# Kernel optimization log

Hardware: AMD Instinct MI355X
Metric: run time of the kernel (lower is better)

The kernel has to match this reference:

```python
import jax, jax.numpy as jnp
import numpy as np

B, S, D, H = 2, 2048, 1024, 16
HD = D // H  # 64
LN_EPS = 1e-5


def setup_inputs() -> dict:
    key = jax.random.key(0)
    ks = jax.random.split(key, 5)
    hidden_states = jax.random.normal(ks[0], (B, S, D), dtype=jnp.float32)
    attention_mask = jnp.zeros((B, 1, 1, S), dtype=jnp.float32)  # additive mask
    # LayerNorm params
    ln_gamma = jnp.ones((D,), dtype=jnp.float32)
    ln_beta = jnp.zeros((D,), dtype=jnp.float32)
    # Q/K/V projections, no bias; stored as [in, out]
    sc = 1.0 / np.sqrt(D)
    Wq = jax.random.normal(ks[1], (D, D), dtype=jnp.float32) * sc
    Wk = jax.random.normal(ks[2], (D, D), dtype=jnp.float32) * sc
    Wv = jax.random.normal(ks[3], (D, D), dtype=jnp.float32) * sc
    return {"hidden_states": hidden_states, "attention_mask": attention_mask,
            "ln_gamma": ln_gamma, "ln_beta": ln_beta, "Wq": Wq, "Wk": Wk, "Wv": Wv}


def _layernorm(x, g, b):
    mu = jnp.mean(x, axis=-1, keepdims=True)
    var = jnp.mean(jnp.square(x - mu), axis=-1, keepdims=True)
    return (x - mu) * jax.lax.rsqrt(var + LN_EPS) * g + b


def reference(hidden_states, attention_mask, ln_gamma, ln_beta, Wq, Wk, Wv):
    h = _layernorm(hidden_states, ln_gamma, ln_beta)          # [B,S,D]
    # project and split heads: [B,S,D] -> [B,H,S,HD]
    def split_heads(x):
        return x.reshape(B, S, H, HD).transpose(0, 2, 1, 3)
    q = split_heads(h @ Wq)
    k = split_heads(h @ Wk)
    v = split_heads(h @ Wv)
    scores = jnp.einsum('bhqd,bhkd->bhqk', q, k) / jnp.sqrt(jnp.float32(HD))
    scores = scores + attention_mask                           # additive mask broadcast
    probs = jax.nn.softmax(scores, axis=-1)                    # dropout p=0 -> identity
    ctx = jnp.einsum('bhqk,bhkd->bhqd', probs, v)              # [B,H,S,HD]
    ctx = ctx.transpose(0, 2, 1, 3).reshape(B, S, H * HD)      # [B,S,D]
    return ctx
```

## Files before the change

### kernel.cpp

```cpp
#include <hip/hip_runtime.h>
#include <hip/hip_bf16.h>
#include <cstdint>

#define B_ 2
#define S_ 2048
#define D_ 1024
#define H_ 16
#define HD_ 64
#define M_ (B_*S_)

#define LOG2E 1.4426950408889634f
#define C1_ (0.125f * LOG2E)

typedef unsigned short u16;
typedef __bf16 bf16x8 __attribute__((ext_vector_type(8)));
typedef u16 u16x8 __attribute__((ext_vector_type(8)));
typedef float f32x4 __attribute__((ext_vector_type(4)));
typedef float f32x16 __attribute__((ext_vector_type(16)));
typedef int i32x4 __attribute__((ext_vector_type(4)));

static __device__ __forceinline__ u16 f2bu(float f) {
  __bf16 b = (__bf16)f;
  return __builtin_bit_cast(unsigned short, b);
}

static __device__ __forceinline__ int cvtpk(float a, float b) {
  int r;
  asm("v_cvt_pk_bf16_f32 %0, %1, %2" : "=v"(r) : "v"(a), "v"(b));
  return r;
}
static __device__ __forceinline__ void plswap(int &x, int &y) {
  asm("v_permlane32_swap_b32 %0, %1" : "+v"(x), "+v"(y));
}

#define GLOAD16(g, l) __builtin_amdgcn_global_load_lds( \
    (__attribute__((address_space(1))) void*)(g), \
    (__attribute__((address_space(3))) void*)(l), 16, 0, 0)

__global__ __launch_bounds__(256) void ln_kernel(const float* __restrict__ x,
    const float* __restrict__ g, const float* __restrict__ be, u16* __restrict__ h) {
  const int row = blockIdx.x;
  const int t = threadIdx.x;
  float4 v = reinterpret_cast<const float4*>(x + (size_t)row * D_)[t];
  float s = v.x + v.y + v.z + v.w;
  float sq = v.x*v.x + v.y*v.y + v.z*v.z + v.w*v.w;
  #pragma unroll
  for (int off = 32; off >= 1; off >>= 1) {
    s  += __shfl_down(s, off);
    sq += __shfl_down(sq, off);
  }
  __shared__ float red[8];
  const int wave = t >> 6, lane = t & 63;
  if (lane == 0) { red[wave] = s; red[4 + wave] = sq; }
  __syncthreads();
  if (t == 0) {
    float ts = red[0]+red[1]+red[2]+red[3];
    float tq = red[4]+red[5]+red[6]+red[7];
    float mu = ts * (1.0f / D_);
    red[0] = mu;
    red[1] = rsqrtf(tq * (1.0f / D_) - mu*mu + 1e-5f);
  }
  __syncthreads();
  const float mu = red[0], rs = red[1];
  float4 gg = reinterpret_cast<const float4*>(g)[t];
  float4 bb = reinterpret_cast<const float4*>(be)[t];
  ushort4 o;
  o.x = f2bu((v.x - mu) * rs * gg.x + bb.x);
  o.y = f2bu((v.y - mu) * rs * gg.y + bb.y);
  o.z = f2bu((v.z - mu) * rs * gg.z + bb.z);
  o.w = f2bu((v.w - mu) * rs * gg.w + bb.w);
  reinterpret_cast<ushort4*>(h + (size_t)row * D_)[t] = o;
}

__global__ __launch_bounds__(256) void wt_kernel(const float* __restrict__ W0,
    const float* __restrict__ W1, const float* __restrict__ W2, u16* __restrict__ wt) {
  const int z = blockIdx.z;
  const float* W = (z == 0) ? W0 : ((z == 1) ? W1 : W2);
  u16* out = wt + (size_t)z * D_ * D_;
  __shared__ float tile[32][33];
  const int n0 = blockIdx.x * 32, k0 = blockIdx.y * 32;
  const int tx = threadIdx.x, ty = threadIdx.y;
  #pragma unroll
  for (int j = 0; j < 4; ++j)
    tile[ty + 8*j][tx] = W[(size_t)(k0 + ty + 8*j) * D_ + n0 + tx];
  __syncthreads();
  #pragma unroll
  for (int j = 0; j < 4; ++j)
    out[(size_t)(n0 + ty + 8*j) * D_ + k0 + tx] = f2bu(tile[tx][ty + 8*j]);
}

__global__ __launch_bounds__(256) void qkv_gemm(const u16* __restrict__ hbuf,
    const u16* __restrict__ wt, u16* __restrict__ qkv) {
  const int z = blockIdx.z;
  const u16* Bt = wt + (size_t)z * D_ * D_;
  u16* outp = qkv + (size_t)z * (B_*H_*S_*HD_);
  __shared__ __align__(16) u16 As[128 * 32];
  __shared__ __align__(16) u16 Bs[128 * 32];
  const int t = threadIdx.x, lane = t & 63, wave = t >> 6;
  const int row0 = blockIdx.y * 128, col0 = blockIdx.x * 128;
  const int wm = wave >> 1, wn = wave & 1;
  f32x4 acc[4][4] = {};
  const int schunk = (t & 3) ^ ((t >> 3) & 3);
  const u16* ag = hbuf + (size_t)(row0 + (t >> 2)) * D_ + schunk * 8;
  const u16* bg = Bt   + (size_t)(col0 + (t >> 2)) * D_ + schunk * 8;
  u16* lA = &As[wave * 512];
  u16* lB = &Bs[wave * 512];
  const char* Ac = (const char*)As;
  const char* Bc = (const char*)Bs;
  const int cbase = (((lane >> 4) ^ ((lane >> 1) & 3)) << 4);

  for (int k0 = 0; k0 < D_; k0 += 32) {
    GLOAD16(ag + k0,           lA);
    GLOAD16(ag + k0 + 64 * D_, lA + 2048);
    GLOAD16(bg + k0,           lB);
    GLOAD16(bg + k0 + 64 * D_, lB + 2048);
    __syncthreads();
    bf16x8 af[4], bfr[4];
    #pragma unroll
    for (int m = 0; m < 4; ++m)
      af[m] = *reinterpret_cast<const bf16x8*>(Ac + (wm*64 + m*16 + (lane & 15)) * 64 + cbase);
    #pragma unroll
    for (int n = 0; n < 4; ++n)
      bfr[n] = *reinterpret_cast<const bf16x8*>(Bc + (wn*64 + n*16 + (lane & 15)) * 64 + cbase);
    #pragma unroll
    for (int m = 0; m < 4; ++m) {
      #pragma unroll
      for (int n = 0; n < 4; ++n)
        acc[m][n] = __builtin_amdgcn_mfma_f32_16x16x32_bf16(af[m], bfr[n], acc[m][n], 0, 0, 0);
    }
    __syncthreads();
  }
  const float scl = (z == 0) ? C1_ : 1.0f;
  #pragma unroll
  for (int m = 0; m < 4; ++m) {
    #pragma unroll
    for (int n = 0; n < 4; ++n) {
      const int gcol = col0 + wn*64 + n*16 + (lane & 15);
      const int hI = gcol >> 6, dI = gcol & 63;
      #pragma unroll
      for (int r = 0; r < 4; ++r) {
        const int grow = row0 + wm*64 + m*16 + (lane >> 4) * 4 + r;
        const int bI = grow >> 11, sI = grow & (S_ - 1);
        size_t idx;
        if (z == 2) idx = ((size_t)(bI * H_ + hI) * HD_ + dI) * S_ + sI;
        else        idx = ((size_t)(bI * H_ + hI) * S_ + sI) * HD_ + dI;
        outp[idx] = f2bu(acc[m][n][r] * scl);
      }
    }
  }
}

static __device__ __forceinline__ void sm_pack(
    const f32x16& s, const float4* __restrict__ mk,
    float& dm, float& lsum, f32x16& o0, f32x16& o1,
    bf16x8& pfA, bf16x8& pfB) {
  float zb[16];
  #pragma unroll
  for (int r = 0; r < 4; ++r) {
    zb[r]      = s[r]      + ((const float*)&mk[0])[r];
    zb[r + 4]  = s[r + 4]  + ((const float*)&mk[1])[r];
    zb[r + 8]  = s[r + 8]  + ((const float*)&mk[2])[r];
    zb[r + 12] = s[r + 12] + ((const float*)&mk[3])[r];
  }
  float a0 = fmaxf(fmaxf(zb[0], zb[1]), zb[2]);
  float a1 = fmaxf(fmaxf(zb[3], zb[4]), zb[5]);
  float a2 = fmaxf(fmaxf(zb[6], zb[7]), zb[8]);
  float a3 = fmaxf(fmaxf(zb[9], zb[10]), zb[11]);
  float a4 = fmaxf(fmaxf(zb[12], zb[13]), zb[14]);
  float tm = fmaxf(fmaxf(fmaxf(a0, a1), fmaxf(a2, a3)), fmaxf(a4, zb[15]));
  if (__builtin_expect(__any(tm > dm + 8.0f), 0)) {
    float tp = fmaxf(tm, __shfl_xor(tm, 32));
    float dnew = fmaxf(dm, tp - 8.0f);
    float sf = __builtin_amdgcn_exp2f(dm - dnew);
    lsum *= sf; o0 = o0 * sf; o1 = o1 * sf; dm = dnew;
  }
  float p[16];
  #pragma unroll
  for (int r = 0; r < 16; ++r) p[r] = __builtin_amdgcn_exp2f(zb[r] - dm);
  float s01 = (p[0] + p[1]) + (p[2] + p[3]);
  float s23 = (p[4] + p[5]) + (p[6] + p[7]);
  float s45 = (p[8] + p[9]) + (p[10] + p[11]);
  float s67 = (p[12] + p[13]) + (p[14] + p[15]);
  lsum += (s01 + s23) + (s45 + s67);
  int pk01 = cvtpk(p[0], p[1]),   pk23 = cvtpk(p[2], p[3]);
  int pk45 = cvtpk(p[4], p[5]),   pk67 = cvtpk(p[6], p[7]);
  int pk89 = cvtpk(p[8], p[9]),   pkAB = cvtpk(p[10], p[11]);
  int pkCD = cvtpk(p[12], p[13]), pkEF = cvtpk(p[14], p[15]);
  plswap(pk01, pk45); plswap(pk23, pk67);
  plswap(pk89, pkCD); plswap(pkAB, pkEF);
  i32x4 c0 = {pk01, pk23, pk45, pk67};
  i32x4 c1 = {pk89, pkAB, pkCD, pkEF};
  pfA = __builtin_bit_cast(bf16x8, c0);
  pfB = __builtin_bit_cast(bf16x8, c1);
}

__global__ __launch_bounds__(256, 2) void attn_kernel(const u16* __restrict__ qkv,
    const float* __restrict__ mask, float* __restrict__ out) {
  const int bid = blockIdx.x;
  const int x = bid & 7, rr = bid >> 3;
  const int j = rr & 15;
  const int pidx = x + ((rr >> 4) << 3);
  const int hI = pidx & 15, bI = pidx >> 4;
  const size_t plane = (size_t)pidx * (S_ * HD_);
  const u16* Qp  = qkv + plane;
  const u16* Kp  = qkv + (size_t)(B_*H_*S_*HD_) + plane;
  const u16* Vtp = qkv + 2*(size_t)(B_*H_*S_*HD_) + plane;

  const int t = threadIdx.x, lane = t & 63, wave = t >> 6;
  const int cl = lane & 31, hf = lane >> 5;
  const int x7 = cl & 7;
  const int hx16 = (hf ^ x7) << 4;
  const int rg = (cl >> 3) * 1056 + x7 * 128;

  __shared__ __align__(16) u16 KsBuf[2][4224];
  __shared__ __align__(16) u16 VsBuf[2][4224];
  __shared__ float maskLds[S_];

  #pragma unroll
  for (int i = 0; i < 2; ++i) {
    float4 mv = reinterpret_cast<const float4*>(mask + (size_t)bI * S_)[t + i*256];
    float4 sm = {mv.x * LOG2E - 8.0f, mv.y * LOG2E - 8.0f,
                 mv.z * LOG2E - 8.0f, mv.w * LOG2E - 8.0f};
    reinterpret_cast<float4*>(maskLds)[t + i*256] = sm;
  }

  const int q0 = j * 128 + wave * 32;
  bf16x8 qf[4];
  #pragma unroll
  for (int d = 0; d < 4; ++d)
    qf[d] = *reinterpret_cast<const bf16x8*>(
        Qp + (size_t)(q0 + cl) * HD_ + d * 16 + hf * 8);

  const int sr = t >> 3;
  const int scol = ((t & 7) ^ ((t >> 3) & 7)) << 3;
  const u16* kSrc = Kp  + (size_t)sr * HD_ + scol;
  const u16* vSrc = Vtp + (size_t)sr * S_  + scol;
  const int dst0 = wave * 528, dst1 = (4 + wave) * 528;

  f32x16 oacc0 = {}, oacc1 = {};
  float dm = 0.f, lsum = 0.f;

  GLOAD16(kSrc,                   &KsBuf[0][dst0]);
  GLOAD16(kSrc + 32 * HD_,        &KsBuf[0][dst1]);
  GLOAD16(vSrc,                   &VsBuf[0][dst0]);
  GLOAD16(vSrc + 32 * (size_t)S_, &VsBuf[0][dst1]);
  int cur = 0;

  for (int kv0 = 0; kv0 < S_; kv0 += 64) {
    __syncthreads();
    if (kv0 + 64 < S_) {
      const u16* kn = kSrc + (size_t)(kv0 + 64) * HD_;
      const u16* vn = vSrc + (kv0 + 64);
      GLOAD16(kn,                   &KsBuf[cur ^ 1][dst0]);
      GLOAD16(kn + 32 * HD_,        &KsBuf[cur ^ 1][dst1]);
      GLOAD16(vn,                   &VsBuf[cur ^ 1][dst0]);
      GLOAD16(vn + 32 * (size_t)S_, &VsBuf[cur ^ 1][dst1]);
    }
    const char* Ks = (const char*)KsBuf[cur];
    const char* Vs = (const char*)VsBuf[cur];

    bf16x8 k0[4], k1[4];
    #pragma unroll
    for (int d = 0; d < 4; ++d) {
      k0[d] = *reinterpret_cast<const bf16x8*>(Ks + rg + ((d << 5) ^ hx16));
      k1[d] = *reinterpret_cast<const bf16x8*>(Ks + rg + 4224 + ((d << 5) ^ hx16));
    }
    float4 mk0[4], mk1[4];
    #pragma unroll
    for (int i = 0; i < 4; ++i) {
      mk0[i] = *reinterpret_cast<const float4*>(&maskLds[kv0 + 8*i + 4*hf]);
      mk1[i] = *reinterpret_cast<const float4*>(&maskLds[kv0 + 32 + 8*i + 4*hf]);
    }
    f32x16 s0 = {}, s1 = {};
    __builtin_amdgcn_s_setprio(1);
    #pragma unroll
    for (int d = 0; d < 4; ++d)
      s0 = __builtin_amdgcn_mfma_f32_32x32x16_bf16(k0[d], qf[d], s0, 0, 0, 0);
    #pragma unroll
    for (int d = 0; d < 4; ++d)
      s1 = __builtin_amdgcn_mfma_f32_32x32x16_bf16(k1[d], qf[d], s1, 0, 0, 0);
    __builtin_amdgcn_s_setprio(0);

    bf16x8 v0[4], v1[4];
    v0[0] = *reinterpret_cast<const bf16x8*>(Vs + rg + (0 ^ hx16));
    v0[1] = *reinterpret_cast<const bf16x8*>(Vs + rg + 4224 + (0 ^ hx16));
    v0[2] = *reinterpret_cast<const bf16x8*>(Vs + rg + (32 ^ hx16));
    v0[3] = *reinterpret_cast<const bf16x8*>(Vs + rg + 4224 + (32 ^ hx16));
    bf16x8 pA, pB;
    sm_pack(s0, mk0, dm, lsum, oacc0, oacc1, pA, pB);
    __builtin_amdgcn_s_setprio(1);
    oacc0 = __builtin_amdgcn_mfma_f32_32x32x16_bf16(v0[0], pA, oacc0, 0, 0, 0);
    oacc1 = __builtin_amdgcn_mfma_f32_32x32x16_bf16(v0[1], pA, oacc1, 0, 0, 0);
    oacc0 = __builtin_amdgcn_mfma_f32_32x32x16_bf16(v0[2], pB, oacc0, 0, 0, 0);
    oacc1 = __builtin_amdgcn_mfma_f32_32x32x16_bf16(v0[3], pB, oacc1, 0, 0, 0);
    __builtin_amdgcn_s_setprio(0);
    v1[0] = *reinterpret_cast<const bf16x8*>(Vs + rg + (64 ^ hx16));
    v1[1] = *reinterpret_cast<const bf16x8*>(Vs + rg + 4224 + (64 ^ hx16));
    v1[2] = *reinterpret_cast<const bf16x8*>(Vs + rg + (96 ^ hx16));
    v1[3] = *reinterpret_cast<const bf16x8*>(Vs + rg + 4224 + (96 ^ hx16));
    sm_pack(s1, mk1, dm, lsum, oacc0, oacc1, pA, pB);
    __builtin_amdgcn_s_setprio(1);
    oacc0 = __builtin_amdgcn_mfma_f32_32x32x16_bf16(v1[0], pA, oacc0, 0, 0, 0);
    oacc1 = __builtin_amdgcn_mfma_f32_32x32x16_bf16(v1[1], pA, oacc1, 0, 0, 0);
    oacc0 = __builtin_amdgcn_mfma_f32_32x32x16_bf16(v1[2], pB, oacc0, 0, 0, 0);
    oacc1 = __builtin_amdgcn_mfma_f32_32x32x16_bf16(v1[3], pB, oacc1, 0, 0, 0);
    __builtin_amdgcn_s_setprio(0);
    cur ^= 1;
  }

  lsum += __shfl_xor(lsum, 32);
  const float rinv = 1.0f / lsum;
  float* orow = out + ((size_t)bI * S_ + q0 + cl) * D_ + hI * HD_;
  #pragma unroll
  for (int jj = 0; jj < 4; ++jj) {
    float4 o0 = {oacc0[4*jj] * rinv, oacc0[4*jj+1] * rinv, oacc0[4*jj+2] * rinv, oacc0[4*jj+3] * rinv};
    float4 o1 = {oacc1[4*jj] * rinv, oacc1[4*jj+1] * rinv, oacc1[4*jj+2] * rinv, oacc1[4*jj+3] * rinv};
    *reinterpret_cast<float4*>(orow + 8*jj + 4*hf)      = o0;
    *reinterpret_cast<float4*>(orow + 32 + 8*jj + 4*hf) = o1;
  }
}

extern "C" void kernel_launch(void* const* d_in, const int* in_sizes, int n_in,
                              void* d_out, int out_size, void* d_ws, size_t ws_size,
                              hipStream_t stream) {
  const float* x     = (const float*)d_in[0];
  const float* mask  = (const float*)d_in[1];
  const float* gamma = (const float*)d_in[2];
  const float* beta  = (const float*)d_in[3];
  const float* Wq    = (const float*)d_in[4];
  const float* Wk    = (const float*)d_in[5];
  const float* Wv    = (const float*)d_in[6];
  float* out = (float*)d_out;

  char* ws = (char*)d_ws;
  u16* hbuf = (u16*)ws;
  u16* wt   = (u16*)(ws + (size_t)M_*D_*2);
  u16* qkv  = (u16*)(ws + (size_t)M_*D_*2 + 3ull*D_*D_*2);

  hipLaunchKernelGGL(ln_kernel, dim3(M_), dim3(256), 0, stream, x, gamma, beta, hbuf);
  hipLaunchKernelGGL(wt_kernel, dim3(32, 32, 3), dim3(32, 8), 0, stream, Wq, Wk, Wv, wt);
  hipLaunchKernelGGL(qkv_gemm, dim3(8, 32, 3), dim3(256), 0, stream, hbuf, wt, qkv);
  hipLaunchKernelGGL(attn_kernel, dim3(512), dim3(256), 0, stream, qkv, mask, out);
}
```

Baseline: 106.9 us.

## Split attention KV range across two wave groups and merge partial softmax results

The attention block grows to 512 threads, made of two 4-wave groups. Each group processes half of the key/value sequence with its own double-buffered LDS tiles held in dynamic shared memory. At the end, group 1 writes its partial accumulators, row sum and max to LDS, and group 0 rescales and merges them before writing the output. This doubles the waves per block so more MFMA and latency-hiding parallelism is available on the 512-block grid, at the cost of more LDS per block (about 74KB), an extra merge step with two barriers, and possibly lower block occupancy.

```diff
diff --git a/kernel.cpp b/kernel.cpp
--- a/kernel.cpp
+++ b/kernel.cpp
@@ -194,8 +194,14 @@
   pfB = __builtin_bit_cast(bf16x8, c1);
 }
 
-__global__ __launch_bounds__(256, 2) void attn_kernel(const u16* __restrict__ qkv,
+__global__ __launch_bounds__(512, 4) void attn_kernel(const u16* __restrict__ qkv,
     const float* __restrict__ mask, float* __restrict__ out) {
+  extern __shared__ __align__(16) char shmem[];
+  char* Kbase = shmem;
+  char* Vbase = shmem + 33792;
+  float* maskLds = (float*)(shmem + 67584);
+  float* comb = (float*)shmem;
+
   const int bid = blockIdx.x;
   const int x = bid & 7, rr = bid >> 3;
   const int j = rr & 15;
@@ -207,57 +213,57 @@
   const u16* Vtp = qkv + 2*(size_t)(B_*H_*S_*HD_) + plane;
 
   const int t = threadIdx.x, lane = t & 63, wave = t >> 6;
+  const int g = wave >> 2, w4 = wave & 3;
   const int cl = lane & 31, hf = lane >> 5;
   const int x7 = cl & 7;
   const int hx16 = (hf ^ x7) << 4;
   const int rg = (cl >> 3) * 1056 + x7 * 128;
 
-  __shared__ __align__(16) u16 KsBuf[2][4224];
-  __shared__ __align__(16) u16 VsBuf[2][4224];
-  __shared__ float maskLds[S_];
-
-  #pragma unroll
-  for (int i = 0; i < 2; ++i) {
-    float4 mv = reinterpret_cast<const float4*>(mask + (size_t)bI * S_)[t + i*256];
+  {
+    float4 mv = reinterpret_cast<const float4*>(mask + (size_t)bI * S_)[t];
     float4 sm = {mv.x * LOG2E - 8.0f, mv.y * LOG2E - 8.0f,
                  mv.z * LOG2E - 8.0f, mv.w * LOG2E - 8.0f};
-    reinterpret_cast<float4*>(maskLds)[t + i*256] = sm;
-  }
-
-  const int q0 = j * 128 + wave * 32;
+    reinterpret_cast<float4*>(maskLds)[t] = sm;
+  }
+
+  const int q0 = j * 128 + w4 * 32;
   bf16x8 qf[4];
   #pragma unroll
   for (int d = 0; d < 4; ++d)
     qf[d] = *reinterpret_cast<const bf16x8*>(
         Qp + (size_t)(q0 + cl) * HD_ + d * 16 + hf * 8);
 
-  const int sr = t >> 3;
-  const int scol = ((t & 7) ^ ((t >> 3) & 7)) << 3;
-  const u16* kSrc = Kp  + (size_t)sr * HD_ + scol;
-  const u16* vSrc = Vtp + (size_t)sr * S_  + scol;
-  const int dst0 = wave * 528, dst1 = (4 + wave) * 528;
+  const int t8 = t & 255;
+  const int sr = t8 >> 3;
+  const int scol = ((t8 & 7) ^ (sr & 7)) << 3;
+  const u16* kSrc = Kp  + (size_t)(g * 1024 + sr) * HD_ + scol;
+  const u16* vSrc = Vtp + (size_t)sr * S_ + g * 1024 + scol;
+  char* kDst = Kbase + g * 16896 + w4 * 1056;
+  char* vDst = Vbase + g * 16896 + w4 * 1056;
 
   f32x16 oacc0 = {}, oacc1 = {};
   float dm = 0.f, lsum = 0.f;
 
-  GLOAD16(kSrc,                   &KsBuf[0][dst0]);
-  GLOAD16(kSrc + 32 * HD_,        &KsBuf[0][dst1]);
-  GLOAD16(vSrc,                   &VsBuf[0][dst0]);
-  GLOAD16(vSrc + 32 * (size_t)S_, &VsBuf[0][dst1]);
+  GLOAD16(kSrc,                   kDst);
+  GLOAD16(kSrc + 32 * HD_,        kDst + 4224);
+  GLOAD16(vSrc,                   vDst);
+  GLOAD16(vSrc + 32 * (size_t)S_, vDst + 4224);
   int cur = 0;
 
-  for (int kv0 = 0; kv0 < S_; kv0 += 64) {
+  for (int kv0 = 0; kv0 < 1024; kv0 += 64) {
     __syncthreads();
-    if (kv0 + 64 < S_) {
+    if (kv0 + 64 < 1024) {
       const u16* kn = kSrc + (size_t)(kv0 + 64) * HD_;
       const u16* vn = vSrc + (kv0 + 64);
-      GLOAD16(kn,                   &KsBuf[cur ^ 1][dst0]);
-      GLOAD16(kn + 32 * HD_,        &KsBuf[cur ^ 1][dst1]);
-      GLOAD16(vn,                   &VsBuf[cur ^ 1][dst0]);
-      GLOAD16(vn + 32 * (size_t)S_, &VsBuf[cur ^ 1][dst1]);
-    }
-    const char* Ks = (const char*)KsBuf[cur];
-    const char* Vs = (const char*)VsBuf[cur];
+      char* kD = kDst + (cur ^ 1) * 8448;
+      char* vD = vDst + (cur ^ 1) * 8448;
+      GLOAD16(kn,                   kD);
+      GLOAD16(kn + 32 * HD_,        kD + 4224);
+      GLOAD16(vn,                   vD);
+      GLOAD16(vn + 32 * (size_t)S_, vD + 4224);
+    }
+    const char* Ks = Kbase + g * 16896 + cur * 8448;
+    const char* Vs = Vbase + g * 16896 + cur * 8448;
 
     bf16x8 k0[4], k1[4];
     #pragma unroll
@@ -265,11 +271,12 @@
       k0[d] = *reinterpret_cast<const bf16x8*>(Ks + rg + ((d << 5) ^ hx16));
       k1[d] = *reinterpret_cast<const bf16x8*>(Ks + rg + 4224 + ((d << 5) ^ hx16));
     }
+    const int gkv = g * 1024 + kv0;
     float4 mk0[4], mk1[4];
     #pragma unroll
     for (int i = 0; i < 4; ++i) {
-      mk0[i] = *reinterpret_cast<const float4*>(&maskLds[kv0 + 8*i + 4*hf]);
-      mk1[i] = *reinterpret_cast<const float4*>(&maskLds[kv0 + 32 + 8*i + 4*hf]);
+      mk0[i] = *reinterpret_cast<const float4*>(&maskLds[gkv + 8*i + 4*hf]);
+      mk1[i] = *reinterpret_cast<const float4*>(&maskLds[gkv + 32 + 8*i + 4*hf]);
     }
     f32x16 s0 = {}, s1 = {};
     __builtin_amdgcn_s_setprio(1);
@@ -309,14 +316,43 @@
   }
 
   lsum += __shfl_xor(lsum, 32);
-  const float rinv = 1.0f / lsum;
-  float* orow = out + ((size_t)bI * S_ + q0 + cl) * D_ + hI * HD_;
-  #pragma unroll
-  for (int jj = 0; jj < 4; ++jj) {
-    float4 o0 = {oacc0[4*jj] * rinv, oacc0[4*jj+1] * rinv, oacc0[4*jj+2] * rinv, oacc0[4*jj+3] * rinv};
-    float4 o1 = {oacc1[4*jj] * rinv, oacc1[4*jj+1] * rinv, oacc1[4*jj+2] * rinv, oacc1[4*jj+3] * rinv};
-    *reinterpret_cast<float4*>(orow + 8*jj + 4*hf)      = o0;
-    *reinterpret_cast<float4*>(orow + 32 + 8*jj + 4*hf) = o1;
+  __syncthreads();
+  const int qw = w4 * 32 + cl;
+  float4* crow = (float4*)(comb + qw * 68);
+  if (g == 1) {
+    #pragma unroll
+    for (int jj = 0; jj < 4; ++jj) {
+      f32x4 a0 = {oacc0[4*jj], oacc0[4*jj+1], oacc0[4*jj+2], oacc0[4*jj+3]};
+      f32x4 a1 = {oacc1[4*jj], oacc1[4*jj+1], oacc1[4*jj+2], oacc1[4*jj+3]};
+      crow[2*jj + hf]     = __builtin_bit_cast(float4, a0);
+      crow[2*jj + hf + 8] = __builtin_bit_cast(float4, a1);
+    }
+    if (hf == 0) { comb[qw*68 + 64] = lsum; comb[qw*68 + 65] = dm; }
+  }
+  __syncthreads();
+  if (g == 0) {
+    const float l1 = comb[qw*68 + 64];
+    const float d1 = comb[qw*68 + 65];
+    const float dd = fmaxf(dm, d1);
+    const float f0 = __builtin_amdgcn_exp2f(dm - dd);
+    const float f1 = __builtin_amdgcn_exp2f(d1 - dd);
+    const float rinv = 1.0f / (lsum * f0 + l1 * f1);
+    float* orow = out + ((size_t)bI * S_ + q0 + cl) * D_ + hI * HD_;
+    #pragma unroll
+    for (int jj = 0; jj < 4; ++jj) {
+      float4 b0 = crow[2*jj + hf];
+      float4 b1 = crow[2*jj + hf + 8];
+      float4 o0 = {(oacc0[4*jj]   * f0 + b0.x * f1) * rinv,
+                   (oacc0[4*jj+1] * f0 + b0.y * f1) * rinv,
+                   (oacc0[4*jj+2] * f0 + b0.z * f1) * rinv,
+                   (oacc0[4*jj+3] * f0 + b0.w * f1) * rinv};
+      float4 o1 = {(oacc1[4*jj]   * f0 + b1.x * f1) * rinv,
+                   (oacc1[4*jj+1] * f0 + b1.y * f1) * rinv,
+                   (oacc1[4*jj+2] * f0 + b1.z * f1) * rinv,
+                   (oacc1[4*jj+3] * f0 + b1.w * f1) * rinv};
+      *reinterpret_cast<float4*>(orow + 8*jj + 4*hf)      = o0;
+      *reinterpret_cast<float4*>(orow + 32 + 8*jj + 4*hf) = o1;
+    }
   }
 }
 
@@ -340,5 +376,5 @@
   hipLaunchKernelGGL(ln_kernel, dim3(M_), dim3(256), 0, stream, x, gamma, beta, hbuf);
   hipLaunchKernelGGL(wt_kernel, dim3(32, 32, 3), dim3(32, 8), 0, stream, Wq, Wk, Wv, wt);
   hipLaunchKernelGGL(qkv_gemm, dim3(8, 32, 3), dim3(256), 0, stream, hbuf, wt, qkv);
-  hipLaunchKernelGGL(attn_kernel, dim3(512), dim3(256), 0, stream, qkv, mask, out);
-}
+  hipLaunchKernelGGL(attn_kernel, dim3(512), dim3(512), 75776, stream, qkv, mask, out);
+}
```

Result: slower. 141.1 us (+32.1%).

## Split attention KV range in two with partial outputs and merge kernel

Applied to the files above, without the earlier changes.

Splits each attention block's 2048-key range into two halves handled by separate blocks, doubling the grid to 1024 blocks and raising the occupancy hint to 4 blocks per CU. The first half writes unnormalized fp32 output plus row max and sum, the second writes bf16 partials into reused workspace, and a new merge kernel combines them. Mask scaling moves to a small prep kernel and is read from global memory rather than LDS. This adds two launches, extra global traffic and bf16 rounding of half the partial sums, in exchange for more parallelism and a shorter per-block loop.

```diff
diff --git a/kernel.cpp b/kernel.cpp
--- a/kernel.cpp
+++ b/kernel.cpp
@@ -23,6 +23,10 @@
   __bf16 b = (__bf16)f;
   return __builtin_bit_cast(unsigned short, b);
 }
+static __device__ __forceinline__ float bu2f(u16 u) {
+  unsigned int v = ((unsigned int)u) << 16;
+  return __builtin_bit_cast(float, v);
+}
 
 static __device__ __forceinline__ int cvtpk(float a, float b) {
   int r;
@@ -36,6 +40,15 @@
 #define GLOAD16(g, l) __builtin_amdgcn_global_load_lds( \
     (__attribute__((address_space(1))) void*)(g), \
     (__attribute__((address_space(3))) void*)(l), 16, 0, 0)
+
+__global__ __launch_bounds__(256) void mask_prep(const float* __restrict__ mask,
+    float* __restrict__ ms) {
+  const int i = blockIdx.x * 256 + threadIdx.x;
+  float4 mv = reinterpret_cast<const float4*>(mask)[i];
+  float4 sm = {mv.x * LOG2E - 8.0f, mv.y * LOG2E - 8.0f,
+               mv.z * LOG2E - 8.0f, mv.w * LOG2E - 8.0f};
+  reinterpret_cast<float4*>(ms)[i] = sm;
+}
 
 __global__ __launch_bounds__(256) void ln_kernel(const float* __restrict__ x,
     const float* __restrict__ g, const float* __restrict__ be, u16* __restrict__ h) {
@@ -194,17 +207,21 @@
   pfB = __builtin_bit_cast(bf16x8, c1);
 }
 
-__global__ __launch_bounds__(256, 2) void attn_kernel(const u16* __restrict__ qkv,
-    const float* __restrict__ mask, float* __restrict__ out) {
+__global__ __launch_bounds__(256, 4) void attn_kernel(const u16* __restrict__ qkv,
+    const float* __restrict__ maskScaled, float* __restrict__ out,
+    u16* __restrict__ part1, float* __restrict__ l0a, float* __restrict__ dm0a,
+    float* __restrict__ l1a, float* __restrict__ dm1a) {
   const int bid = blockIdx.x;
   const int x = bid & 7, rr = bid >> 3;
-  const int j = rr & 15;
-  const int pidx = x + ((rr >> 4) << 3);
+  const int w = rr & 31;
+  const int pidx = x + ((rr >> 5) << 3);
+  const int j = w & 15, g = w >> 4;
   const int hI = pidx & 15, bI = pidx >> 4;
   const size_t plane = (size_t)pidx * (S_ * HD_);
   const u16* Qp  = qkv + plane;
   const u16* Kp  = qkv + (size_t)(B_*H_*S_*HD_) + plane;
   const u16* Vtp = qkv + 2*(size_t)(B_*H_*S_*HD_) + plane;
+  const float* maskS = maskScaled + (size_t)bI * S_ + g * 1024;
 
   const int t = threadIdx.x, lane = t & 63, wave = t >> 6;
   const int cl = lane & 31, hf = lane >> 5;
@@ -214,15 +231,6 @@
 
   __shared__ __align__(16) u16 KsBuf[2][4224];
   __shared__ __align__(16) u16 VsBuf[2][4224];
-  __shared__ float maskLds[S_];
-
-  #pragma unroll
-  for (int i = 0; i < 2; ++i) {
-    float4 mv = reinterpret_cast<const float4*>(mask + (size_t)bI * S_)[t + i*256];
-    float4 sm = {mv.x * LOG2E - 8.0f, mv.y * LOG2E - 8.0f,
-                 mv.z * LOG2E - 8.0f, mv.w * LOG2E - 8.0f};
-    reinterpret_cast<float4*>(maskLds)[t + i*256] = sm;
-  }
 
   const int q0 = j * 128 + wave * 32;
   bf16x8 qf[4];
@@ -232,9 +240,9 @@
         Qp + (size_t)(q0 + cl) * HD_ + d * 16 + hf * 8);
 
   const int sr = t >> 3;
-  const int scol = ((t & 7) ^ ((t >> 3) & 7)) << 3;
-  const u16* kSrc = Kp  + (size_t)sr * HD_ + scol;
-  const u16* vSrc = Vtp + (size_t)sr * S_  + scol;
+  const int scol = ((t & 7) ^ (sr & 7)) << 3;
+  const u16* kSrc = Kp  + (size_t)(g * 1024 + sr) * HD_ + scol;
+  const u16* vSrc = Vtp + (size_t)sr * S_ + g * 1024 + scol;
   const int dst0 = wave * 528, dst1 = (4 + wave) * 528;
 
   f32x16 oacc0 = {}, oacc1 = {};
@@ -246,9 +254,9 @@
   GLOAD16(vSrc + 32 * (size_t)S_, &VsBuf[0][dst1]);
   int cur = 0;
 
-  for (int kv0 = 0; kv0 < S_; kv0 += 64) {
+  for (int kv0 = 0; kv0 < 1024; kv0 += 64) {
     __syncthreads();
-    if (kv0 + 64 < S_) {
+    if (kv0 + 64 < 1024) {
       const u16* kn = kSrc + (size_t)(kv0 + 64) * HD_;
       const u16* vn = vSrc + (kv0 + 64);
       GLOAD16(kn,                   &KsBuf[cur ^ 1][dst0]);
@@ -268,8 +276,8 @@
     float4 mk0[4], mk1[4];
     #pragma unroll
     for (int i = 0; i < 4; ++i) {
-      mk0[i] = *reinterpret_cast<const float4*>(&maskLds[kv0 + 8*i + 4*hf]);
-      mk1[i] = *reinterpret_cast<const float4*>(&maskLds[kv0 + 32 + 8*i + 4*hf]);
+      mk0[i] = *reinterpret_cast<const float4*>(&maskS[kv0 + 8*i + 4*hf]);
+      mk1[i] = *reinterpret_cast<const float4*>(&maskS[kv0 + 32 + 8*i + 4*hf]);
     }
     f32x16 s0 = {}, s1 = {};
     __builtin_amdgcn_s_setprio(1);
@@ -309,15 +317,53 @@
   }
 
   lsum += __shfl_xor(lsum, 32);
-  const float rinv = 1.0f / lsum;
-  float* orow = out + ((size_t)bI * S_ + q0 + cl) * D_ + hI * HD_;
-  #pragma unroll
-  for (int jj = 0; jj < 4; ++jj) {
-    float4 o0 = {oacc0[4*jj] * rinv, oacc0[4*jj+1] * rinv, oacc0[4*jj+2] * rinv, oacc0[4*jj+3] * rinv};
-    float4 o1 = {oacc1[4*jj] * rinv, oacc1[4*jj+1] * rinv, oacc1[4*jj+2] * rinv, oacc1[4*jj+3] * rinv};
-    *reinterpret_cast<float4*>(orow + 8*jj + 4*hf)      = o0;
-    *reinterpret_cast<float4*>(orow + 32 + 8*jj + 4*hf) = o1;
-  }
+  const int row = pidx * S_ + q0 + cl;
+  if (g == 0) {
+    float* orow = out + ((size_t)bI * S_ + q0 + cl) * D_ + hI * HD_;
+    #pragma unroll
+    for (int jj = 0; jj < 4; ++jj) {
+      float4 o0 = {oacc0[4*jj], oacc0[4*jj+1], oacc0[4*jj+2], oacc0[4*jj+3]};
+      float4 o1 = {oacc1[4*jj], oacc1[4*jj+1], oacc1[4*jj+2], oacc1[4*jj+3]};
+      *reinterpret_cast<float4*>(orow + 8*jj + 4*hf)      = o0;
+      *reinterpret_cast<float4*>(orow + 32 + 8*jj + 4*hf) = o1;
+    }
+    if (hf == 0) { l0a[row] = lsum; dm0a[row] = dm; }
+  } else {
+    u16* prow = part1 + (size_t)row * HD_;
+    #pragma unroll
+    for (int jj = 0; jj < 4; ++jj) {
+      ushort4 u0 = {f2bu(oacc0[4*jj]), f2bu(oacc0[4*jj+1]), f2bu(oacc0[4*jj+2]), f2bu(oacc0[4*jj+3])};
+      ushort4 u1 = {f2bu(oacc1[4*jj]), f2bu(oacc1[4*jj+1]), f2bu(oacc1[4*jj+2]), f2bu(oacc1[4*jj+3])};
+      *reinterpret_cast<ushort4*>(prow + 8*jj + 4*hf)      = u0;
+      *reinterpret_cast<ushort4*>(prow + 32 + 8*jj + 4*hf) = u1;
+    }
+    if (hf == 0) { l1a[row] = lsum; dm1a[row] = dm; }
+  }
+}
+
+__global__ __launch_bounds__(256) void merge_kernel(float* __restrict__ out,
+    const u16* __restrict__ part1, const float* __restrict__ l0a,
+    const float* __restrict__ dm0a, const float* __restrict__ l1a,
+    const float* __restrict__ dm1a) {
+  const int e = blockIdx.x * 256 + threadIdx.x;
+  const int row = e >> 4;
+  const int d4 = (e & 15) << 2;
+  const int pidx = row >> 11, q = row & (S_ - 1);
+  const int bI = pidx >> 4, hI = pidx & 15;
+  const float dm0 = dm0a[row], dm1 = dm1a[row];
+  const float dd = fmaxf(dm0, dm1);
+  const float f0 = __builtin_amdgcn_exp2f(dm0 - dd);
+  const float f1 = __builtin_amdgcn_exp2f(dm1 - dd);
+  const float rinv = 1.0f / (l0a[row] * f0 + l1a[row] * f1);
+  float* op = out + ((size_t)bI * S_ + q) * D_ + hI * HD_ + d4;
+  float4 o0 = *reinterpret_cast<const float4*>(op);
+  ushort4 u1 = *reinterpret_cast<const ushort4*>(part1 + (size_t)row * HD_ + d4);
+  float4 r;
+  r.x = (o0.x * f0 + bu2f(u1.x) * f1) * rinv;
+  r.y = (o0.y * f0 + bu2f(u1.y) * f1) * rinv;
+  r.z = (o0.z * f0 + bu2f(u1.z) * f1) * rinv;
+  r.w = (o0.w * f0 + bu2f(u1.w) * f1) * rinv;
+  *reinterpret_cast<float4*>(op) = r;
 }
 
 extern "C" void kernel_launch(void* const* d_in, const int* in_sizes, int n_in,
@@ -334,11 +380,23 @@
 
   char* ws = (char*)d_ws;
   u16* hbuf = (u16*)ws;
-  u16* wt   = (u16*)(ws + (size_t)M_*D_*2);
+  char* wtb = ws + (size_t)M_*D_*2;
+  u16* wt   = (u16*)wtb;
   u16* qkv  = (u16*)(ws + (size_t)M_*D_*2 + 3ull*D_*D_*2);
-
+  float* maskScaled = (float*)(ws + (size_t)M_*D_*2 + 3ull*D_*D_*2 + 3ull*B_*H_*S_*HD_*2);
+
+  u16* part1 = hbuf;
+  float* l0a  = (float*)wtb;
+  float* dm0a = (float*)(wtb + (1u<<18));
+  float* l1a  = (float*)(wtb + (2u<<18));
+  float* dm1a = (float*)(wtb + (3u<<18));
+
+  hipLaunchKernelGGL(mask_prep, dim3(4), dim3(256), 0, stream, mask, maskScaled);
   hipLaunchKernelGGL(ln_kernel, dim3(M_), dim3(256), 0, stream, x, gamma, beta, hbuf);
   hipLaunchKernelGGL(wt_kernel, dim3(32, 32, 3), dim3(32, 8), 0, stream, Wq, Wk, Wv, wt);
   hipLaunchKernelGGL(qkv_gemm, dim3(8, 32, 3), dim3(256), 0, stream, hbuf, wt, qkv);
-  hipLaunchKernelGGL(attn_kernel, dim3(512), dim3(256), 0, stream, qkv, mask, out);
-}
+  hipLaunchKernelGGL(attn_kernel, dim3(1024), dim3(256), 0, stream, qkv, maskScaled,
+                     out, part1, l0a, dm0a, l1a, dm1a);
+  hipLaunchKernelGGL(merge_kernel, dim3(4096), dim3(256), 0, stream, out, part1,
+                     l0a, dm0a, l1a, dm1a);
+}
```

New measurement: 170.8 us. 59.9% more time.
